# Kernel tuning notes

Hardware: AMD Instinct MI355X
Metric: run time of the kernel (lower is better)

Reference implementation:

```python
import jax, jax.numpy as jnp
import numpy as np

N, H, K, B, L = 8192, 256, 128, 64, 128


def setup_inputs() -> dict:
    key = jax.random.key(0)
    ks = jax.random.split(key, 12)
    s_emb = 1.0 / np.sqrt(H)
    return {
        "A": jax.random.normal(ks[0], (N, N), jnp.float32) * 0.02,           # dense adjacency
        "emb": jax.random.normal(ks[1], (N, H), jnp.float32) * s_emb,        # GCN embedding
        "Wc": jax.random.normal(ks[2], (H, H), jnp.float32) * s_emb,         # Conv1d k=1 (multi_gram)
        "bc": jnp.zeros((H,), jnp.float32),
        "W1": jax.random.normal(ks[3], (K, 2 * H), jnp.float32) * 0.05,      # Conv2d fs=1, width=2H
        "b1": jnp.zeros((K,), jnp.float32),
        "W2": jax.random.normal(ks[4], (K, 2, 2 * H), jnp.float32) * 0.05,   # Conv2d fs=2
        "b2": jnp.zeros((K,), jnp.float32),
        "Wd": jax.random.normal(ks[5], (2, 4 * K), jnp.float32) * 0.05,      # dense
        "bd": jnp.zeros((2,), jnp.float32),
        "q_idx": jax.random.randint(ks[6], (B, L), 0, N, jnp.int32),
        "a_idx": jax.random.randint(ks[7], (B, L), 0, N, jnp.int32),
    }


def reference(A, emb, Wc, bc, W1, b1, W2, b2, Wd, bd, q_idx, a_idx):
    # GCN layer (featureless): layer1 = A @ embedding  -> [N, H]
    layer1 = A @ emb

    # padded per-sample word gather + multi_gram (kernel-1 conv == rowwise linear + ReLU)
    def gram(idx):
        x = jnp.take(layer1, idx, axis=0)                      # [B, L, H]
        return jax.nn.relu(jnp.einsum("blh,oh->blo", x, Wc) + bc)

    Qm = gram(q_idx)                                           # [B, L, H]
    Am = gram(a_idx)                                           # [B, L, H]

    # soft cross attention
    s = jnp.einsum("bqh,bkh->bqk", Qm, Am)                     # [B, Lq, La]
    eq = jnp.einsum("bqk,bkh->bqh", jax.nn.softmax(s, axis=-1), Am)
    ea = jnp.einsum("bkq,bqh->bkh", jax.nn.softmax(jnp.swapaxes(s, 1, 2), axis=-1), Qm)

    # full-width conv2d encoders over [L, 2H] feature map, max-pooled over L
    def encode(X, E):
        t = jnp.concatenate([(X - E) ** 2, X * E], axis=-1)    # [B, L, 2H]
        e1 = jax.nn.relu(jnp.einsum("bld,kd->blk", t, W1) + b1).max(axis=1)      # fs=1 -> [B, K]
        e2 = jax.nn.relu(
            jnp.einsum("bld,kd->blk", t[:, :-1], W2[:, 0])
            + jnp.einsum("bld,kd->blk", t[:, 1:], W2[:, 1])
            + b2
        ).max(axis=1)                                          # fs=2 -> [B, K]
        return jax.nn.relu(jnp.concatenate([e1, e2], axis=-1)) # [B, 2K] (dropout = identity in eval)

    re = jnp.concatenate([encode(Qm, eq), encode(Am, ea)], axis=-1)  # [B, 4K]
    return jax.nn.log_softmax(re @ Wd.T + bd, axis=-1)          # [B, 2]
```

## Files before the change

kernel.cpp:

```cpp
#include <hip/hip_runtime.h>
#include <hip/hip_bf16.h>
#include <math.h>

#define NN 8192
#define HH 256
#define BB 64
#define LL 128
#define SPLITK 4

typedef __attribute__((ext_vector_type(8))) short short8v;
typedef __attribute__((ext_vector_type(4))) short short4v;
typedef __attribute__((ext_vector_type(4))) float f32x4;

static __device__ inline short bf16bits(float f) {
    __hip_bfloat16 h = __float2bfloat16(f);
    return __builtin_bit_cast(short, h);
}
static __device__ inline float bits2f(short s) {
    __hip_bfloat16 h = __builtin_bit_cast(__hip_bfloat16, s);
    return __bfloat162float(h);
}
static __device__ inline short8v cvt8(float4 f0, float4 f1) {
    short8v r;
    r[0] = bf16bits(f0.x); r[1] = bf16bits(f0.y);
    r[2] = bf16bits(f0.z); r[3] = bf16bits(f0.w);
    r[4] = bf16bits(f1.x); r[5] = bf16bits(f1.y);
    r[6] = bf16bits(f1.z); r[7] = bf16bits(f1.w);
    return r;
}
static __device__ inline void glds16(const void* src, void* lds) {
    __builtin_amdgcn_global_load_lds(
        (const __attribute__((address_space(1))) void*)src,
        (__attribute__((address_space(3))) void*)lds, 16, 0, 0);
}
template<int N> static __device__ inline void vmwait() {
    if constexpr (N == 0)  asm volatile("s_waitcnt vmcnt(0)"  ::: "memory");
    else if constexpr (N == 1)  asm volatile("s_waitcnt vmcnt(1)"  ::: "memory");
    else if constexpr (N == 2)  asm volatile("s_waitcnt vmcnt(2)"  ::: "memory");
    else if constexpr (N == 3)  asm volatile("s_waitcnt vmcnt(3)"  ::: "memory");
    else if constexpr (N == 4)  asm volatile("s_waitcnt vmcnt(4)"  ::: "memory");
    else if constexpr (N == 5)  asm volatile("s_waitcnt vmcnt(5)"  ::: "memory");
    else if constexpr (N == 6)  asm volatile("s_waitcnt vmcnt(6)"  ::: "memory");
    else if constexpr (N == 7)  asm volatile("s_waitcnt vmcnt(7)"  ::: "memory");
    else if constexpr (N == 8)  asm volatile("s_waitcnt vmcnt(8)"  ::: "memory");
    else                        asm volatile("s_waitcnt vmcnt(12)" ::: "memory");
}
static __device__ inline void lgkm0_barrier() {
    asm volatile("s_waitcnt lgkmcnt(0)" ::: "memory");
    __builtin_amdgcn_s_barrier();
    __builtin_amdgcn_sched_barrier(0);
}


__global__ __launch_bounds__(256) void prep(
    const float* __restrict__ emb, short* __restrict__ embT,
    const float* __restrict__ Wc, short* __restrict__ Wcb,
    const float* __restrict__ W1, const float* __restrict__ W2,
    short* __restrict__ WcatT)
{
    __shared__ short tile[64][65];
    const int bid = blockIdx.x;
    const int t = threadIdx.x;
    if (bid < 512) {
        const int k0 = (bid & 127) * 64, h0 = (bid >> 7) * 64;
#pragma unroll
        for (int i = 0; i < 16; i++) {
            int idx = t + i * 256;
            int k = idx >> 6, h = idx & 63;
            tile[h][k] = bf16bits(emb[(long)(k0 + k) * 256 + h0 + h]);
        }
        __syncthreads();
#pragma unroll
        for (int i = 0; i < 16; i++) {
            int idx = t + i * 256;
            int h = idx >> 6, k = idx & 63;
            int n = h0 + h;
            int kk = (k0 + k) ^ ((n & 3) << 3);
            embT[(long)n * NN + kk] = tile[h][k];
        }
    } else {
        int i = (bid - 512) * 256 + t;
        if (i < 256 * 256) {
            int n = i >> 8, c = i & 255;
            Wcb[n * 256 + (c ^ ((n & 3) << 3))] = bf16bits(Wc[i]);
        }
        if (i < 384 * 512) {
            int n = i >> 9, d = i & 511;
            float v;
            if (n < 128)      v = W1[n * 512 + d];
            else if (n < 256) v = W2[(n - 128) * 1024 + d];
            else              v = W2[(n - 256) * 1024 + 512 + d];
            WcatT[n * 512 + (d ^ ((n & 3) << 3))] = bf16bits(v);
        }
    }
}

__global__ __launch_bounds__(512, 2) void l1_gemm(
    const float* __restrict__ Af, const short* __restrict__ Bt,
    short* __restrict__ Part)
{
    constexpr int AST = 40;

    __shared__ short As[4][128 * AST];
    __shared__ short Bs[4][256 * 32];

    const int tid = threadIdx.x;
    const int wave = tid >> 6, lane = tid & 63;
    const int wr = wave >> 2, wc = wave & 3;
    const int r16 = lane & 15, kg = lane >> 4;

    const int sk = blockIdx.x & 3, mt = blockIdx.x >> 2;
    const int m0 = mt * 128;
    const int kbeg = sk * 2048;
    constexpr int NIT = 64;

    const int arow = tid >> 2;
    const int akc = (tid & 3) * 8;
    const long arow_g = (long)(m0 + arow) * NN;

    f32x4 acc[4][4] = {};

#define STAGE_B(T, BUF)                                                        \
    {                                                                          \
        const int kt_ = kbeg + (T) * 32;                                       \
        _Pragma("unroll")                                                      \
        for (int c = 0; c < 2; c++) {                                          \
            int chunk = c * 512 + tid;                                         \
            int n_ = chunk >> 2, kc_ = (chunk & 3) * 8;                        \
            glds16(Bt + (long)n_ * NN + kt_ + kc_,                             \
                   &Bs[BUF][(c * 512 + wave * 64) * 8]);                       \
        }                                                                      \
    }
#define LOAD_A(T, F0, F1)                                                      \
    {                                                                          \
        const float* ap_ = Af + arow_g + kbeg + (T) * 32 + akc;                \
        (F0) = *(const float4*)ap_; (F1) = *(const float4*)(ap_ + 4);          \
    }
#define WRITE_A(BUF, F0, F1) { *(short8v*)&As[BUF][arow * AST + akc] = cvt8((F0), (F1)); }

    float4 p0f0, p0f1, c1f0, c1f1, c2f0, c2f1;
    LOAD_A(0, p0f0, p0f1);  STAGE_B(0, 0);
    LOAD_A(1, c1f0, c1f1);  STAGE_B(1, 1);
    LOAD_A(2, c2f0, c2f1);  STAGE_B(2, 2);
    WRITE_A(0, p0f0, p0f1);
    vmwait<8>();
    lgkm0_barrier();

    for (int t = 0; t < NIT; ++t) {
        const int cur = t & 3, nw = (t + 1) & 3, ns = (t + 3) & 3;
        float4 nf0, nf1;
        if (t + 3 < NIT) {
            LOAD_A(t + 3, nf0, nf1);
            STAGE_B(t + 3, ns);
        }

        short8v a[4], b[4];
#pragma unroll
        for (int i = 0; i < 4; i++)
            a[i] = *(const short8v*)&As[cur][(wr * 64 + i * 16 + r16) * AST + kg * 8];
#pragma unroll
        for (int j = 0; j < 4; j++) {
            int n = wc * 64 + j * 16 + r16;
            b[j] = *(const short8v*)&Bs[cur][n * 32 + ((kg * 8) ^ ((n & 3) << 3))];
        }
#pragma unroll
        for (int i = 0; i < 4; i++)
#pragma unroll
            for (int j = 0; j < 4; j++)
                acc[i][j] = __builtin_amdgcn_mfma_f32_16x16x32_bf16(
                    a[i], b[j], acc[i][j], 0, 0, 0);

        if (t + 1 < NIT) {
            WRITE_A(nw, c1f0, c1f1);
            if (t + 3 < NIT)      vmwait<8>();
            else if (t + 2 < NIT) vmwait<4>();
            else                  vmwait<0>();
            lgkm0_barrier();
        }
        c1f0 = c2f0; c1f1 = c2f1;
        c2f0 = nf0;  c2f1 = nf1;
    }
#undef STAGE_B
#undef LOAD_A
#undef WRITE_A

    short* P = Part + (long)sk * NN * HH;
#pragma unroll
    for (int i = 0; i < 4; i++)
#pragma unroll
        for (int j = 0; j < 4; j++) {
            int col = wc * 64 + j * 16 + r16;
#pragma unroll
            for (int r = 0; r < 4; r++) {
                int row = m0 + wr * 64 + i * 16 + kg * 4 + r;
                P[(long)row * HH + col] = bf16bits(acc[i][j][r]);
            }
        }
}

__global__ __launch_bounds__(256) void reduceK(
    const short* __restrict__ P, short* __restrict__ out)
{
    const long n = (long)NN * HH;
    long i = ((long)blockIdx.x * 256 + threadIdx.x) * 8;
    if (i >= n) return;
    float acc[8] = {};
#pragma unroll
    for (int k = 0; k < SPLITK; k++) {
        short8v v = *(const short8v*)&P[(long)k * n + i];
#pragma unroll
        for (int j = 0; j < 8; j++) acc[j] += bits2f(v[j]);
    }
    short8v o;
#pragma unroll
    for (int j = 0; j < 8; j++) o[j] = bf16bits(acc[j]);
    *(short8v*)&out[i] = o;
}

template<int NW, int NT, int GATHER, int EPI>
__global__ __launch_bounds__(256) void gemm_small(
    const short* __restrict__ Aq, const short* __restrict__ Aa,
    const short* __restrict__ Bt,
    float* __restrict__ Cfq, float* __restrict__ Cfa,
    short* __restrict__ Cbq, short* __restrict__ Cba,
    short* __restrict__ Ctq, short* __restrict__ Cta,
    const float* __restrict__ bias,
    const int* __restrict__ idxq, const int* __restrict__ idxa,
    int M, int N, int Kd)
{
    constexpr int BM = 64;
    constexpr int BN = NW * 4;
    constexpr int NB = NW / 16;
    constexpr int BCALLS = BN / BM;
    constexpr int OPS = 1 + BCALLS;
    constexpr int AST = 40;

    __shared__ short As[4][BM * AST];
    __shared__ short Bs[4][BN * 32];

    const int tid = threadIdx.x;
    const int wave = tid >> 6, lane = tid & 63;
    const int wc = wave & 3;
    const int r16 = lane & 15, kg = lane >> 4;

    const int bid = blockIdx.x;
    const int side = bid & 1;
    const int nt = (bid >> 1) & (NT - 1);
    const int mt = bid >> (NT == 2 ? 2 : 1);
    const int m0 = mt * BM;
    const int n0 = nt * BN;
    const int niter = Kd / 32;

    const short* Ab = side ? Aa : Aq;
    const int* rowidx = side ? idxa : idxq;

    const int arow = tid >> 2;
    const int akc = (tid & 3) * 8;
    long arow_g;
    { int r = GATHER ? rowidx[m0 + arow] : (m0 + arow); arow_g = (long)r * Kd; }

    f32x4 acc[4][NB] = {};

#define STAGE_B(T, BUF)                                                        \
    {                                                                          \
        const int kt_ = (T) * 32;                                              \
        _Pragma("unroll")                                                      \
        for (int c = 0; c < BCALLS; c++) {                                     \
            int chunk = c * 256 + tid;                                         \
            int n_ = chunk >> 2, kc_ = (chunk & 3) * 8;                        \
            glds16(Bt + (long)(n0 + n_) * Kd + kt_ + kc_,                      \
                   &Bs[BUF][(c * 256 + wave * 64) * 8]);                       \
        }                                                                      \
    }
#define LOAD_A(T, AR)  { (AR) = *(const short8v*)(Ab + arow_g + (T) * 32 + akc); }
#define WRITE_A(BUF, AR) { *(short8v*)&As[BUF][arow * AST + akc] = (AR); }

    short8v a0, a1, a2;
    LOAD_A(0, a0);  STAGE_B(0, 0);
    LOAD_A(1, a1);  STAGE_B(1, 1);
    LOAD_A(2, a2);  STAGE_B(2, 2);
    WRITE_A(0, a0);
    vmwait<2 * OPS>();
    lgkm0_barrier();

    for (int t = 0; t < niter; ++t) {
        const int cur = t & 3, nw = (t + 1) & 3, ns = (t + 3) & 3;
        short8v na;
        if (t + 3 < niter) {
            LOAD_A(t + 3, na);
            STAGE_B(t + 3, ns);
        }

        short8v a[4], b[NB];
#pragma unroll
        for (int i = 0; i < 4; i++)
            a[i] = *(const short8v*)&As[cur][(i * 16 + r16) * AST + kg * 8];
#pragma unroll
        for (int j = 0; j < NB; j++) {
            int n = wc * NW + j * 16 + r16;
            b[j] = *(const short8v*)&Bs[cur][n * 32 + ((kg * 8) ^ ((n & 3) << 3))];
        }
#pragma unroll
        for (int i = 0; i < 4; i++)
#pragma unroll
            for (int j = 0; j < NB; j++)
                acc[i][j] = __builtin_amdgcn_mfma_f32_16x16x32_bf16(
                    a[i], b[j], acc[i][j], 0, 0, 0);

        if (t + 1 < niter) {
            WRITE_A(nw, a1);
            if (t + 3 < niter)      vmwait<2 * OPS>();
            else if (t + 2 < niter) vmwait<OPS>();
            else                    vmwait<0>();
            lgkm0_barrier();
        }
        a1 = a2; a2 = na;
    }
#undef STAGE_B
#undef LOAD_A
#undef WRITE_A

    if (EPI == 2) {
        float* Cf = side ? Cfa : Cfq;
#pragma unroll
        for (int i = 0; i < 4; i++)
#pragma unroll
            for (int j = 0; j < NB; j++) {
                int col = n0 + wc * NW + j * 16 + r16;
#pragma unroll
                for (int r = 0; r < 4; r++) {
                    int row = m0 + i * 16 + kg * 4 + r;
                    Cf[(long)row * N + col] = acc[i][j][r];
                }
            }
    } else {
        short* Cb = side ? Cba : Cbq;
        short* Ct = side ? Cta : Ctq;
#pragma unroll
        for (int i = 0; i < 4; i++)
#pragma unroll
            for (int j = 0; j < NB; j++) {
                int col = n0 + wc * NW + j * 16 + r16;
                float bv = bias[col];
                float vr[4];
#pragma unroll
                for (int r = 0; r < 4; r++)
                    vr[r] = fmaxf(acc[i][j][r] + bv, 0.f);
                int rbase = m0 + i * 16 + kg * 4;
                int bb = rbase >> 7;
                int lbase = rbase & 127;
#pragma unroll
                for (int r = 0; r < 4; r++) {
                    int grow = rbase + r;
                    Cb[(long)grow * 256 + (col ^ ((grow & 7) << 3))] = bf16bits(vr[r]);
                }
                short4v t4;
#pragma unroll
                for (int r = 0; r < 4; r++) t4[r] = bf16bits(vr[r]);
                int lsw = lbase ^ ((col & 7) << 3);
                *(short4v*)&Ct[(long)bb * (256 * 128) + col * 128 + lsw] = t4;
            }
    }
}

__global__ __launch_bounds__(256) void qkT(
    const short* __restrict__ Qb16, const short* __restrict__ Ab16,
    float* __restrict__ s)
{
    __shared__ short Q[64 * 256];
    __shared__ short Am[128 * 256];
    const int b = blockIdx.x >> 1;
    const int qh = blockIdx.x & 1;
    const int tid = threadIdx.x, wave = tid >> 6, lane = tid & 63;
    const int r16 = lane & 15, kg = lane >> 4;
    const long boff = (long)b * 128 * 256;
    const long qoff = boff + (long)qh * 64 * 256;

#pragma unroll
    for (int c = 0; c < 8; c++)
        glds16(Qb16 + qoff + ((long)c * 256 + tid) * 8, &Q[(c * 256 + wave * 64) * 8]);
#pragma unroll
    for (int c = 0; c < 16; c++)
        glds16(Ab16 + boff + ((long)c * 256 + tid) * 8, &Am[(c * 256 + wave * 64) * 8]);
    __syncthreads();

    f32x4 acc[8] = {};
    const int q0 = wave * 16;
#pragma unroll
    for (int ks = 0; ks < 8; ks++) {
        short8v a;
        {
            int q = q0 + r16;
            a = *(const short8v*)&Q[q * 256 + ((ks * 32 + kg * 8) ^ ((q & 7) << 3))];
        }
#pragma unroll
        for (int j = 0; j < 8; j++) {
            int n = j * 16 + r16;
            short8v bf = *(const short8v*)&Am[n * 256 + ((ks * 32 + kg * 8) ^ ((n & 7) << 3))];
            acc[j] = __builtin_amdgcn_mfma_f32_16x16x32_bf16(a, bf, acc[j], 0, 0, 0);
        }
    }

    float* sp = s + (long)b * 16384 + (long)qh * 64 * 128;
#pragma unroll
    for (int j = 0; j < 8; j++)
#pragma unroll
        for (int r = 0; r < 4; r++) {
            int q = q0 + kg * 4 + r;
            int k = j * 16 + r16;
            sp[q * 128 + k] = acc[j][r];
        }
}

__global__ __launch_bounds__(256) void attn_pv(
    const float* __restrict__ s,
    const short* __restrict__ AT, const short* __restrict__ QT,
    const short* __restrict__ Qb16, const short* __restrict__ Ab16,
    short* __restrict__ t_q, short* __restrict__ t_a)
{
    __shared__ float sm[128 * 128];
    __shared__ short P[128 * 128];
    short* XL = (short*)sm;
    const int b = blockIdx.x >> 1;
    const int side = blockIdx.x & 1;
    const int tid = threadIdx.x, wave = tid >> 6, lane = tid & 63;
    const int r16 = lane & 15, kg = lane >> 4;

    const short* XT   = side ? QT : AT;
    const short* Xrow = side ? Ab16 : Qb16;
    short* tout       = side ? t_a : t_q;

#pragma unroll
    for (int c = 0; c < 16; c++)
        glds16(s + (long)b * 16384 + ((long)c * 256 + tid) * 4,
               &sm[(c * 256 + wave * 64) * 4]);
    __syncthreads();

    {
        const int r = tid >> 1;
        const int base = (tid & 1) * 64;
        float mx = -1e30f;
#pragma unroll 8
        for (int i = 0; i < 64; i++) {
            int k = base + ((i + r) & 63);
            float v = side ? sm[k * 128 + r] : sm[r * 128 + k];
            mx = fmaxf(mx, v);
        }
        mx = fmaxf(mx, __shfl_xor(mx, 1));
        float sum = 0.f;
#pragma unroll 8
        for (int i = 0; i < 64; i++) {
            int k = base + ((i + r) & 63);
            float v = side ? sm[k * 128 + r] : sm[r * 128 + k];
            sum += __expf(v - mx);
        }
        sum += __shfl_xor(sum, 1);
        float inv = 1.f / sum;
#pragma unroll 8
        for (int i = 0; i < 64; i++) {
            int k = base + ((i + r) & 63);
            float v = side ? sm[k * 128 + r] : sm[r * 128 + k];
            P[r * 128 + (k ^ ((r & 7) << 3))] = bf16bits(__expf(v - mx) * inv);
        }
    }
    __syncthreads();

#pragma unroll
    for (int c = 0; c < 16; c++)
        glds16(XT + (long)b * 32768 + ((long)c * 256 + tid) * 8,
               &XL[(c * 256 + wave * 64) * 8]);
    __syncthreads();

    f32x4 acc[8][4] = {};
#pragma unroll
    for (int ks = 0; ks < 4; ks++) {
        short8v a[8], bf[4];
#pragma unroll
        for (int i = 0; i < 8; i++) {
            int row = i * 16 + r16;
            a[i] = *(const short8v*)&P[row * 128 + ((ks * 32 + kg * 8) ^ ((row & 7) << 3))];
        }
#pragma unroll
        for (int j = 0; j < 4; j++) {
            int h = wave * 64 + j * 16 + r16;
            bf[j] = *(const short8v*)&XL[h * 128 + ((ks * 32 + kg * 8) ^ ((h & 7) << 3))];
        }
#pragma unroll
        for (int i = 0; i < 8; i++)
#pragma unroll
            for (int j = 0; j < 4; j++)
                acc[i][j] = __builtin_amdgcn_mfma_f32_16x16x32_bf16(
                    a[i], bf[j], acc[i][j], 0, 0, 0);
    }

    short* tp = tout + (long)b * 128 * 512;
    const short* xr = Xrow + (long)b * 128 * 256;
#pragma unroll
    for (int i = 0; i < 8; i++)
#pragma unroll
        for (int j = 0; j < 4; j++) {
            int col = wave * 64 + j * 16 + r16;
#pragma unroll
            for (int r = 0; r < 4; r++) {
                int row = i * 16 + kg * 4 + r;
                float E = acc[i][j][r];
                float x = bits2f(xr[row * 256 + (col ^ ((row & 7) << 3))]);
                float d = x - E;
                tp[(long)row * 512 + col] = bf16bits(d * d);
                tp[(long)row * 512 + 256 + col] = bf16bits(x * E);
            }
        }
}

__global__ __launch_bounds__(512) void pool_final(
    const float* __restrict__ u_q, const float* __restrict__ u_a,
    const float* __restrict__ b1, const float* __restrict__ b2,
    const float* __restrict__ Wd, const float* __restrict__ bd,
    float* __restrict__ out)
{
    __shared__ float re[512];
    const int b = blockIdx.x;
    const int t = threadIdx.x;
    const int side = t >> 8;
    const int kk = t & 255;
    const float* uu = side ? u_a : u_q;
    if (kk < 128) {
        int k = kk;
        float bias = b1[k];
        float mx = -1e30f;
        for (int l = 0; l < 128; l++) {
            float v = uu[((long)b * 128 + l) * 384 + k] + bias;
            mx = fmaxf(mx, v);
        }
        re[side * 256 + k] = fmaxf(mx, 0.f);
    } else {
        int k = kk - 128;
        float bias = b2[k];
        float mx = -1e30f;
        for (int l = 0; l < 127; l++) {
            float v = uu[((long)b * 128 + l) * 384 + 128 + k]
                    + uu[((long)b * 128 + l + 1) * 384 + 256 + k] + bias;
            mx = fmaxf(mx, v);
        }
        re[side * 256 + 128 + k] = fmaxf(mx, 0.f);
    }
    __syncthreads();
    if (t < 64) {
        float p0 = 0.f, p1 = 0.f;
        for (int d = t; d < 512; d += 64) {
            float r = re[d];
            p0 = fmaf(r, Wd[d], p0);
            p1 = fmaf(r, Wd[512 + d], p1);
        }
#pragma unroll
        for (int off = 32; off; off >>= 1) {
            p0 += __shfl_xor(p0, off);
            p1 += __shfl_xor(p1, off);
        }
        if (t == 0) {
            float l0 = p0 + bd[0], l1 = p1 + bd[1];
            float m = fmaxf(l0, l1);
            float lse = m + logf(expf(l0 - m) + expf(l1 - m));
            out[b * 2 + 0] = l0 - lse;
            out[b * 2 + 1] = l1 - lse;
        }
    }
}

extern "C" void kernel_launch(void* const* d_in, const int* in_sizes, int n_in,
                              void* d_out, int out_size, void* d_ws, size_t ws_size,
                              hipStream_t stream)
{
    const float* A    = (const float*)d_in[0];
    const float* emb  = (const float*)d_in[1];
    const float* Wc   = (const float*)d_in[2];
    const float* bc   = (const float*)d_in[3];
    const float* W1   = (const float*)d_in[4];
    const float* b1   = (const float*)d_in[5];
    const float* W2   = (const float*)d_in[6];
    const float* b2   = (const float*)d_in[7];
    const float* Wd   = (const float*)d_in[8];
    const float* bd   = (const float*)d_in[9];
    const int* q_idx  = (const int*)d_in[10];
    const int* a_idx  = (const int*)d_in[11];
    float* out = (float*)d_out;
    float* ws  = (float*)d_ws;

    const long SZ_L1 = (long)NN * HH;
    float* p      = ws;
    short* Part   = (short*)p;          p += (long)SPLITK * SZ_L1 / 2;
    short* l1b    = (short*)p;          p += SZ_L1 / 2 + 1024;
    short* Wcb    = (short*)p;          p += 32768 + 1024;
    short* WcatT  = (short*)p;          p += 98304 + 1024;
    short* embT   = (short*)p;          p += SZ_L1 / 2 + 1024;
    short* Qb16   = (short*)p;          p += SZ_L1 / 2 + 1024;
    short* Ab16   = (short*)p;          p += SZ_L1 / 2 + 1024;
    short* QT     = (short*)p;          p += SZ_L1 / 2 + 1024;
    short* AT     = (short*)p;          p += SZ_L1 / 2 + 1024;
    float* s      = p;                  p += (long)BB * LL * LL;
    short* t_q    = (short*)p;          p += SZ_L1 + 1024;
    short* t_a    = (short*)p;          p += SZ_L1 + 1024;
    float* u_q    = p;                  p += (long)BB * LL * 384;
    float* u_a    = p;                  p += (long)BB * LL * 384;

    prep<<<1280, 256, 0, stream>>>(emb, embT, Wc, Wcb, W1, W2, WcatT);

    l1_gemm<<<256, 512, 0, stream>>>(A, embT, Part);
    reduceK<<<(int)(SZ_L1 / 8 / 256), 256, 0, stream>>>(Part, l1b);

    gemm_small<32, 2, 1, 1><<<512, 256, 0, stream>>>(
        l1b, l1b, Wcb, nullptr, nullptr, Qb16, Ab16, QT, AT, bc,
        q_idx, a_idx, BB * LL, HH, HH);

    qkT<<<2 * BB, 256, 0, stream>>>(Qb16, Ab16, s);
    attn_pv<<<2 * BB, 256, 0, stream>>>(s, AT, QT, Qb16, Ab16, t_q, t_a);

    gemm_small<48, 2, 0, 2><<<512, 256, 0, stream>>>(
        t_q, t_a, WcatT, u_q, u_a, nullptr, nullptr, nullptr, nullptr, nullptr,
        nullptr, nullptr, BB * LL, 384, 512);

    pool_final<<<BB, 512, 0, stream>>>(u_q, u_a, b1, b2, Wd, bd, out);
}
```

Measured before the change: 200.2 us.

## Shrink l1_gemm pipeline buffers for occupancy and split attn_pv rows across blocks

The l1_gemm prefetch depth drops from 3 stages to 2, with 2 A buffers and 3 B buffers, to cut LDS use, and the launch bound asks for 4 blocks per CU. attn_pv now splits each (batch, side) into two 64-row halves, giving 4*B blocks. It also issues the XT load at the same time as the score load so they overlap. The tighter launch bound limits per-thread registers, which can cause spills in the MFMA accumulator-heavy GEMM. The grid of 256 blocks may not benefit from higher occupancy anyway, and the shallower prefetch exposes more memory latency.

Result: faster. 176.3 us, median of 3 (-12.0%).

```diff
diff --git a/kernel.cpp b/kernel.cpp
--- a/kernel.cpp
+++ b/kernel.cpp
@@ -95,14 +95,14 @@
     }
 }
 
-__global__ __launch_bounds__(512, 2) void l1_gemm(
+__global__ __launch_bounds__(512, 4) void l1_gemm(
     const float* __restrict__ Af, const short* __restrict__ Bt,
     short* __restrict__ Part)
 {
     constexpr int AST = 40;
 
-    __shared__ short As[4][128 * AST];
-    __shared__ short Bs[4][256 * 32];
+    __shared__ short As[2][128 * AST];
+    __shared__ short Bs[3][256 * 32];
 
     const int tid = threadIdx.x;
     const int wave = tid >> 6, lane = tid & 63;
@@ -138,30 +138,30 @@
     }
 #define WRITE_A(BUF, F0, F1) { *(short8v*)&As[BUF][arow * AST + akc] = cvt8((F0), (F1)); }
 
-    float4 p0f0, p0f1, c1f0, c1f1, c2f0, c2f1;
+    float4 p0f0, p0f1, c1f0, c1f1;
     LOAD_A(0, p0f0, p0f1);  STAGE_B(0, 0);
     LOAD_A(1, c1f0, c1f1);  STAGE_B(1, 1);
-    LOAD_A(2, c2f0, c2f1);  STAGE_B(2, 2);
     WRITE_A(0, p0f0, p0f1);
-    vmwait<8>();
+    vmwait<4>();
     lgkm0_barrier();
 
     for (int t = 0; t < NIT; ++t) {
-        const int cur = t & 3, nw = (t + 1) & 3, ns = (t + 3) & 3;
+        const int curA = t & 1, nwA = (t + 1) & 1;
+        const int curB = t % 3, nsB = (t + 2) % 3;
         float4 nf0, nf1;
-        if (t + 3 < NIT) {
-            LOAD_A(t + 3, nf0, nf1);
-            STAGE_B(t + 3, ns);
+        if (t + 2 < NIT) {
+            LOAD_A(t + 2, nf0, nf1);
+            STAGE_B(t + 2, nsB);
         }
 
         short8v a[4], b[4];
 #pragma unroll
         for (int i = 0; i < 4; i++)
-            a[i] = *(const short8v*)&As[cur][(wr * 64 + i * 16 + r16) * AST + kg * 8];
+            a[i] = *(const short8v*)&As[curA][(wr * 64 + i * 16 + r16) * AST + kg * 8];
 #pragma unroll
         for (int j = 0; j < 4; j++) {
             int n = wc * 64 + j * 16 + r16;
-            b[j] = *(const short8v*)&Bs[cur][n * 32 + ((kg * 8) ^ ((n & 3) << 3))];
+            b[j] = *(const short8v*)&Bs[curB][n * 32 + ((kg * 8) ^ ((n & 3) << 3))];
         }
 #pragma unroll
         for (int i = 0; i < 4; i++)
@@ -171,14 +171,12 @@
                     a[i], b[j], acc[i][j], 0, 0, 0);
 
         if (t + 1 < NIT) {
-            WRITE_A(nw, c1f0, c1f1);
-            if (t + 3 < NIT)      vmwait<8>();
-            else if (t + 2 < NIT) vmwait<4>();
-            else                  vmwait<0>();
+            WRITE_A(nwA, c1f0, c1f1);
+            if (t + 2 < NIT) vmwait<4>();
+            else             vmwait<0>();
             lgkm0_barrier();
         }
-        c1f0 = c2f0; c1f1 = c2f1;
-        c2f0 = nf0;  c2f1 = nf1;
+        c1f0 = nf0; c1f1 = nf1;
     }
 #undef STAGE_B
 #undef LOAD_A
@@ -418,11 +416,12 @@
     const short* __restrict__ Qb16, const short* __restrict__ Ab16,
     short* __restrict__ t_q, short* __restrict__ t_a)
 {
-    __shared__ float sm[128 * 128];
-    __shared__ short P[128 * 128];
-    short* XL = (short*)sm;
-    const int b = blockIdx.x >> 1;
-    const int side = blockIdx.x & 1;
+    __shared__ short XL[256 * 128];
+    __shared__ float sm[64 * 128];
+    __shared__ short P[64 * 128];
+    const int b = blockIdx.x >> 2;
+    const int side = (blockIdx.x >> 1) & 1;
+    const int h = blockIdx.x & 1;
     const int tid = threadIdx.x, wave = tid >> 6, lane = tid & 63;
     const int r16 = lane & 15, kg = lane >> 4;
 
@@ -432,71 +431,81 @@
 
 #pragma unroll
     for (int c = 0; c < 16; c++)
-        glds16(s + (long)b * 16384 + ((long)c * 256 + tid) * 4,
-               &sm[(c * 256 + wave * 64) * 4]);
+        glds16(XT + (long)b * 32768 + ((long)c * 256 + tid) * 8,
+               &XL[(c * 256 + wave * 64) * 8]);
+    if (side == 0) {
+#pragma unroll
+        for (int c = 0; c < 8; c++)
+            glds16(s + (long)b * 16384 + (long)h * 8192 + ((long)c * 256 + tid) * 4,
+                   &sm[(c * 256 + wave * 64) * 4]);
+    } else {
+#pragma unroll
+        for (int c = 0; c < 8; c++) {
+            int idx = c * 256 + tid;
+            int q = idx >> 4, off = (idx & 15) * 4;
+            glds16(s + (long)b * 16384 + (long)q * 128 + h * 64 + off,
+                   &sm[(c * 256 + wave * 64) * 4]);
+        }
+    }
     __syncthreads();
 
     {
-        const int r = tid >> 1;
-        const int base = (tid & 1) * 64;
+        const int r = tid >> 2;
+        const int qt = tid & 3;
         float mx = -1e30f;
 #pragma unroll 8
-        for (int i = 0; i < 64; i++) {
-            int k = base + ((i + r) & 63);
-            float v = side ? sm[k * 128 + r] : sm[r * 128 + k];
+        for (int i = 0; i < 32; i++) {
+            int k = qt * 32 + ((i + r) & 31);
+            float v = (side == 0) ? sm[r * 128 + k] : sm[k * 64 + r];
             mx = fmaxf(mx, v);
         }
         mx = fmaxf(mx, __shfl_xor(mx, 1));
+        mx = fmaxf(mx, __shfl_xor(mx, 2));
         float sum = 0.f;
 #pragma unroll 8
-        for (int i = 0; i < 64; i++) {
-            int k = base + ((i + r) & 63);
-            float v = side ? sm[k * 128 + r] : sm[r * 128 + k];
+        for (int i = 0; i < 32; i++) {
+            int k = qt * 32 + ((i + r) & 31);
+            float v = (side == 0) ? sm[r * 128 + k] : sm[k * 64 + r];
             sum += __expf(v - mx);
         }
         sum += __shfl_xor(sum, 1);
+        sum += __shfl_xor(sum, 2);
         float inv = 1.f / sum;
 #pragma unroll 8
-        for (int i = 0; i < 64; i++) {
-            int k = base + ((i + r) & 63);
-            float v = side ? sm[k * 128 + r] : sm[r * 128 + k];
+        for (int i = 0; i < 32; i++) {
+            int k = qt * 32 + ((i + r) & 31);
+            float v = (side == 0) ? sm[r * 128 + k] : sm[k * 64 + r];
             P[r * 128 + (k ^ ((r & 7) << 3))] = bf16bits(__expf(v - mx) * inv);
         }
     }
     __syncthreads();
 
-#pragma unroll
-    for (int c = 0; c < 16; c++)
-        glds16(XT + (long)b * 32768 + ((long)c * 256 + tid) * 8,
-               &XL[(c * 256 + wave * 64) * 8]);
-    __syncthreads();
-
-    f32x4 acc[8][4] = {};
+    f32x4 acc[4][4] = {};
 #pragma unroll
     for (int ks = 0; ks < 4; ks++) {
-        short8v a[8], bf[4];
-#pragma unroll
-        for (int i = 0; i < 8; i++) {
+        short8v a[4], bf[4];
+#pragma unroll
+        for (int i = 0; i < 4; i++) {
             int row = i * 16 + r16;
             a[i] = *(const short8v*)&P[row * 128 + ((ks * 32 + kg * 8) ^ ((row & 7) << 3))];
         }
 #pragma unroll
         for (int j = 0; j < 4; j++) {
-            int h = wave * 64 + j * 16 + r16;
-            bf[j] = *(const short8v*)&XL[h * 128 + ((ks * 32 + kg * 8) ^ ((h & 7) << 3))];
-        }
-#pragma unroll
-        for (int i = 0; i < 8; i++)
+            int hh = wave * 64 + j * 16 + r16;
+            bf[j] = *(const short8v*)&XL[hh * 128 + ((ks * 32 + kg * 8) ^ ((hh & 7) << 3))];
+        }
+#pragma unroll
+        for (int i = 0; i < 4; i++)
 #pragma unroll
             for (int j = 0; j < 4; j++)
                 acc[i][j] = __builtin_amdgcn_mfma_f32_16x16x32_bf16(
                     a[i], bf[j], acc[i][j], 0, 0, 0);
     }
 
-    short* tp = tout + (long)b * 128 * 512;
-    const short* xr = Xrow + (long)b * 128 * 256;
-#pragma unroll
-    for (int i = 0; i < 8; i++)
+    short* tp = tout + (long)b * 128 * 512 + (long)h * 64 * 512;
+    const short* xr = Xrow + (long)b * 128 * 256 + (long)h * 64 * 256;
+#pragma unroll
+    for (int i = 0; i < 4; i++)
 #pragma unroll
         for (int j = 0; j < 4; j++) {
             int col = wave * 64 + j * 16 + r16;
@@ -613,7 +622,7 @@
         q_idx, a_idx, BB * LL, HH, HH);
 
     qkT<<<2 * BB, 256, 0, stream>>>(Qb16, Ab16, s);
-    attn_pv<<<2 * BB, 256, 0, stream>>>(s, AT, QT, Qb16, Ab16, t_q, t_a);
+    attn_pv<<<4 * BB, 256, 0, stream>>>(s, AT, QT, Qb16, Ab16, t_q, t_a);
 
     gemm_small<48, 2, 0, 2><<<512, 256, 0, stream>>>(
         t_q, t_a, WcatT, u_q, u_a, nullptr, nullptr, nullptr, nullptr, nullptr,
```
